# Performance work log

Measured on AMD Instinct MI355X. Metric: run time of the kernel, lower is better.

Reference implementation:

```python
import jax, jax.numpy as jnp
import numpy as np

HID = 1024
NH = 4  # heads for GAT conv1 and all attention blocks
FF = 2048
SLOPE = 0.2


def _ln(x, g, b):
    m = x.mean(-1, keepdims=True)
    v = ((x - m) ** 2).mean(-1, keepdims=True)
    return (x - m) / jnp.sqrt(v + 1e-5) * g + b


def _mha(q, k, v, in_w, in_b, out_w, out_b, nh):
    # q:[B,Lq,E], k/v:[B,Lk,E]; torch MultiheadAttention math (eval mode)
    B, Lq, E = q.shape
    hd = E // nh
    wq, wk, wv = jnp.split(in_w, 3, axis=0)
    bq, bk, bv = jnp.split(in_b, 3)
    qh = (q @ wq.T + bq).reshape(B, Lq, nh, hd)
    kh = (k @ wk.T + bk).reshape(B, -1, nh, hd)
    vh = (v @ wv.T + bv).reshape(B, -1, nh, hd)
    s = jnp.einsum('bqhd,bkhd->bhqk', qh, kh) / jnp.sqrt(jnp.asarray(hd, q.dtype))
    a = jax.nn.softmax(s, axis=-1)
    o = jnp.einsum('bhqk,bkhd->bqhd', a, vh).reshape(B, Lq, E)
    return o @ out_w.T + out_b


def _gatv2(x, edge_index, w_l, b_l, w_r, b_r, att, bias, heads, out_ch):
    # PyG GATv2Conv, flow='target_to_source': i (aggregation dst) = edge_index[0], j = edge_index[1]
    n = x.shape[0]
    dst = edge_index[0]
    src = edge_index[1]
    x_l = (x @ w_l + b_l).reshape(n, heads, out_ch)
    x_r = (x @ w_r + b_r).reshape(n, heads, out_ch)
    msg = x_l[src]                                   # [E,H,C] gathered source features
    e = jax.nn.leaky_relu(msg + x_r[dst], SLOPE)     # [E,H,C]
    alpha = (e * att).sum(-1)                        # [E,H]
    amax = jax.ops.segment_max(alpha, dst, num_segments=n)
    alpha = jnp.exp(alpha - amax[dst])
    denom = jax.ops.segment_sum(alpha, dst, num_segments=n)
    alpha = alpha / (denom[dst] + 1e-16)
    out = jax.ops.segment_sum(msg * alpha[..., None], dst, num_segments=n)
    return out.reshape(n, heads * out_ch) + bias


def setup_inputs() -> dict:
    key = jax.random.key(0)
    ks = iter(jax.random.split(key, 64))
    N, DF, B, L, E_rand = 8000, 768, 32, 14, 96000
    w = lambda *s: jax.random.normal(next(ks), s, jnp.float32) * 0.02
    z = lambda *s: jnp.zeros(s, jnp.float32)
    o = lambda *s: jnp.ones(s, jnp.float32)
    ei = jax.random.randint(next(ks), (2, E_rand), 0, N, jnp.int32)
    self_loops = jnp.tile(jnp.arange(N, dtype=jnp.int32)[None, :], (2, 1))
    inp = {
        'img_feat': jax.random.normal(next(ks), (B, HID), jnp.float32),
        'node_features': jax.random.normal(next(ks), (N, DF), jnp.float32),
        'edge_index': jnp.concatenate([ei, self_loops], axis=1),
        'target_idx': jax.random.randint(next(ks), (L,), 0, N, jnp.int32),
        # GATv2 conv1: 768 -> 4 heads x 256
        'gat1_wl': w(DF, HID), 'gat1_bl': z(HID), 'gat1_wr': w(DF, HID), 'gat1_br': z(HID),
        'gat1_att': w(NH, HID // NH), 'gat1_bias': z(HID),
        # GATv2 conv2: 1024 -> 1 head x 1024
        'gat2_wl': w(HID, HID), 'gat2_bl': z(HID), 'gat2_wr': w(HID, HID), 'gat2_br': z(HID),
        'gat2_att': w(1, HID), 'gat2_bias': z(HID),
        # cross-modal MHA + FFN layer
        'xa_in_w': w(3 * HID, HID), 'xa_in_b': z(3 * HID), 'xa_out_w': w(HID, HID), 'xa_out_b': z(HID),
        'xl_l1_w': w(FF, HID), 'xl_l1_b': z(FF), 'xl_l2_w': w(HID, FF), 'xl_l2_b': z(HID),
        'xl_n1_g': o(HID), 'xl_n1_b': z(HID), 'xl_n2_g': o(HID), 'xl_n2_b': z(HID),
        # 2-layer TransformerEncoder (stacked leading dim = layer)
        'enc_in_w': w(2, 3 * HID, HID), 'enc_in_b': z(2, 3 * HID),
        'enc_out_w': w(2, HID, HID), 'enc_out_b': z(2, HID),
        'enc_l1_w': w(2, FF, HID), 'enc_l1_b': z(2, FF),
        'enc_l2_w': w(2, HID, FF), 'enc_l2_b': z(2, HID),
        'enc_n1_g': o(2, HID), 'enc_n1_b': z(2, HID),
        'enc_n2_g': o(2, HID), 'enc_n2_b': z(2, HID),
        'cls_w': w(1, HID), 'cls_b': z(1),
    }
    return inp


def reference(img_feat, node_features, edge_index, target_idx,
              gat1_wl, gat1_bl, gat1_wr, gat1_br, gat1_att, gat1_bias,
              gat2_wl, gat2_bl, gat2_wr, gat2_br, gat2_att, gat2_bias,
              xa_in_w, xa_in_b, xa_out_w, xa_out_b,
              xl_l1_w, xl_l1_b, xl_l2_w, xl_l2_b, xl_n1_g, xl_n1_b, xl_n2_g, xl_n2_b,
              enc_in_w, enc_in_b, enc_out_w, enc_out_b, enc_l1_w, enc_l1_b, enc_l2_w, enc_l2_b,
              enc_n1_g, enc_n1_b, enc_n2_g, enc_n2_b, cls_w, cls_b):
    x = _gatv2(node_features, edge_index, gat1_wl, gat1_bl, gat1_wr, gat1_br, gat1_att, gat1_bias, NH, HID // NH)
    x = jax.nn.leaky_relu(x, SLOPE)
    x = _gatv2(x, edge_index, gat2_wl, gat2_bl, gat2_wr, gat2_br, gat2_att, gat2_bias, 1, HID)
    t = x[target_idx]                                  # [L, HID]
    B = img_feat.shape[0]
    L = t.shape[0]
    q = jnp.broadcast_to(t[None], (B, L, HID))
    kv = img_feat[:, None, :]                          # [B, 1, HID]
    attn = _mha(q, kv, kv, xa_in_w, xa_in_b, xa_out_w, xa_out_b, NH)
    src = _ln(t[None] + attn, xl_n1_g, xl_n1_b)
    ff = jax.nn.relu(src @ xl_l1_w.T + xl_l1_b) @ xl_l2_w.T + xl_l2_b
    src = _ln(src + ff, xl_n2_g, xl_n2_b)
    for i in range(2):  # TransformerEncoder, post-norm, relu, eval mode
        a = _mha(src, src, src, enc_in_w[i], enc_in_b[i], enc_out_w[i], enc_out_b[i], NH)
        src = _ln(src + a, enc_n1_g[i], enc_n1_b[i])
        f = jax.nn.relu(src @ enc_l1_w[i].T + enc_l1_b[i]) @ enc_l2_w[i].T + enc_l2_b[i]
        src = _ln(src + f, enc_n2_g[i], enc_n2_b[i])
    return (src @ cls_w.T + cls_b)[..., 0]             # [B, L]
```

## Files before the change

kernel.cpp:

```cpp
#include <hip/hip_runtime.h>
#include <hip/hip_bf16.h>

typedef __bf16 bf16;
typedef bf16 bf16x8 __attribute__((ext_vector_type(8)));
typedef bf16 bf16x4 __attribute__((ext_vector_type(4)));
typedef float f32x4 __attribute__((ext_vector_type(4)));

#define HID 1024
#define FFD 2048

typedef __attribute__((address_space(3))) void lds_void;
typedef const __attribute__((address_space(1))) void gm_void;

__device__ __forceinline__ void gload_lds16(const bf16* g, bf16* l)
{
    __builtin_amdgcn_global_load_lds((gm_void*)g, (lds_void*)l, 16, 0, 0);
}

__global__ __launch_bounds__(256) void cvt_bf16_kernel(
    const float* __restrict__ src, bf16* __restrict__ dst, long n)
{
    long i = ((long)blockIdx.x * 256 + threadIdx.x) * 4;
    if (i >= n) return;
    float4 f = *(const float4*)&src[i];
    bf16x4 v = {(bf16)f.x, (bf16)f.y, (bf16)f.z, (bf16)f.w};
    *(bf16x4*)&dst[i] = v;
}

__global__ __launch_bounds__(256) void cvt_t_bf16_kernel(
    const float* __restrict__ in, bf16* __restrict__ out, int R, int C)
{
    __shared__ bf16 tile[32][33];
    const int c0 = blockIdx.x * 32, r0 = blockIdx.y * 32;
    const int tx = threadIdx.x & 31, ty = threadIdx.x >> 5;
#pragma unroll
    for (int i = ty; i < 32; i += 8)
        tile[i][tx] = (bf16)in[(long)(r0 + i) * C + c0 + tx];
    __syncthreads();
#pragma unroll
    for (int i = ty; i < 32; i += 8)
        out[(long)(c0 + i) * R + r0 + tx] = tile[tx][i];
}

template <int ACT, int OUTBF16>
__global__ __launch_bounds__(256) void gemm_bf16_kernel(
    const bf16* __restrict__ A, const bf16* __restrict__ B,
    const float* __restrict__ bias, void* __restrict__ Cp,
    int M, int N, int K, int NB)
{
    const int total = gridDim.x;
    const int h = blockIdx.x;
    const int t = (total % 8 == 0) ? ((h & 7) * (total >> 3) + (h >> 3)) : h;
    const int bn = t % NB, bm = t / NB;

    const int tid  = threadIdx.x;
    const int lane = tid & 63, wave = tid >> 6;
    const int wr   = wave >> 1, wc = wave & 1;

    __shared__ bf16 As[128][32];
    __shared__ bf16 Bs[128][32];

    f32x4 acc[4][4] = {};

    const int srow = wave * 16 + (lane >> 2);
    const int scol = (lane & 3) << 3;
    const long ga0 = (long)min(bm * 128 + srow,      M - 1) * K + scol;
    const long ga1 = (long)min(bm * 128 + srow + 64, M - 1) * K + scol;
    const long gb0 = (long)(bn * 128 + srow)      * K + scol;
    const long gb1 = (long)(bn * 128 + srow + 64) * K + scol;
    bf16* ldsA0 = &As[0][0] + wave * 512;
    bf16* ldsA1 = &As[0][0] + 2048 + wave * 512;
    bf16* ldsB0 = &Bs[0][0] + wave * 512;
    bf16* ldsB1 = &Bs[0][0] + 2048 + wave * 512;

    const int quad = lane >> 4;
    const int mr   = lane & 15;
    const int kf   = quad * 8;

    for (int k0 = 0; k0 < K; k0 += 32) {
        gload_lds16(A + ga0 + k0, ldsA0);
        gload_lds16(A + ga1 + k0, ldsA1);
        gload_lds16(B + gb0 + k0, ldsB0);
        gload_lds16(B + gb1 + k0, ldsB1);
        __syncthreads();

        bf16x8 af[4], bfr[4];
#pragma unroll
        for (int i = 0; i < 4; ++i) af[i]  = *(const bf16x8*)&As[wr * 64 + i * 16 + mr][kf];
#pragma unroll
        for (int j = 0; j < 4; ++j) bfr[j] = *(const bf16x8*)&Bs[wc * 64 + j * 16 + mr][kf];
#pragma unroll
        for (int i = 0; i < 4; ++i)
#pragma unroll
            for (int j = 0; j < 4; ++j)
                acc[i][j] = __builtin_amdgcn_mfma_f32_16x16x32_bf16(af[i], bfr[j], acc[i][j], 0, 0, 0);
        __syncthreads();
    }

    const int crow = quad * 4;
#pragma unroll
    for (int i = 0; i < 4; ++i) {
#pragma unroll
        for (int j = 0; j < 4; ++j) {
            const int   col = bn * 128 + wc * 64 + j * 16 + mr;
            const float bv  = bias[col];
#pragma unroll
            for (int r = 0; r < 4; ++r) {
                const int row = bm * 128 + wr * 64 + i * 16 + crow + r;
                if (row < M) {
                    float v = acc[i][j][r] + bv;
                    if (ACT == 1) v = fmaxf(v, 0.f);
                    if (OUTBF16) ((bf16*)Cp)[(long)row * N + col] = (bf16)v;
                    else         ((float*)Cp)[(long)row * N + col] = v;
                }
            }
        }
    }
}

template <int KS>
__global__ __launch_bounds__(256) void gemm_sk_kernel(
    const float* __restrict__ A, const float* __restrict__ Bt,
    float* __restrict__ part, int M, int N, int K)
{
    const int tid  = threadIdx.x;
    const int bn   = blockIdx.x, bm = blockIdx.y, kz = blockIdx.z;
    const int lane = tid & 63, wave = tid >> 6;
    const int wr   = wave >> 1, wc = wave & 1;

    __shared__ bf16 As[128][40];
    __shared__ bf16 Bs[128][40];

    f32x4 acc[4][4] = {};

    const int  lr = tid >> 2;
    const int  lc = (tid & 3) << 3;
    const long a0 = (long)min(bm * 128 + lr,      M - 1) * K;
    const long a1 = (long)min(bm * 128 + lr + 64, M - 1) * K;
    const long b0 = (long)(bn * 128 + lr)      * K;
    const long b1 = (long)(bn * 128 + lr + 64) * K;

    const int quad = lane >> 4;
    const int mr   = lane & 15;
    const int kf   = quad * 8;

    const int Kc   = K / KS;
    const int kbeg = kz * Kc, kend = kbeg + Kc;

    float4 ra[4], rb[4];
    auto load_chunk = [&](int k0) {
        ra[0] = *(const float4*)&A[a0 + k0 + lc];
        ra[1] = *(const float4*)&A[a0 + k0 + lc + 4];
        ra[2] = *(const float4*)&A[a1 + k0 + lc];
        ra[3] = *(const float4*)&A[a1 + k0 + lc + 4];
        rb[0] = *(const float4*)&Bt[b0 + k0 + lc];
        rb[1] = *(const float4*)&Bt[b0 + k0 + lc + 4];
        rb[2] = *(const float4*)&Bt[b1 + k0 + lc];
        rb[3] = *(const float4*)&Bt[b1 + k0 + lc + 4];
    };

    load_chunk(kbeg);
    for (int k0 = kbeg; k0 < kend; k0 += 32) {
        {
            bf16x8 v0 = {(bf16)ra[0].x,(bf16)ra[0].y,(bf16)ra[0].z,(bf16)ra[0].w,
                         (bf16)ra[1].x,(bf16)ra[1].y,(bf16)ra[1].z,(bf16)ra[1].w};
            *(bf16x8*)&As[lr][lc] = v0;
            bf16x8 v1 = {(bf16)ra[2].x,(bf16)ra[2].y,(bf16)ra[2].z,(bf16)ra[2].w,
                         (bf16)ra[3].x,(bf16)ra[3].y,(bf16)ra[3].z,(bf16)ra[3].w};
            *(bf16x8*)&As[lr + 64][lc] = v1;
            bf16x8 v2 = {(bf16)rb[0].x,(bf16)rb[0].y,(bf16)rb[0].z,(bf16)rb[0].w,
                         (bf16)rb[1].x,(bf16)rb[1].y,(bf16)rb[1].z,(bf16)rb[1].w};
            *(bf16x8*)&Bs[lr][lc] = v2;
            bf16x8 v3 = {(bf16)rb[2].x,(bf16)rb[2].y,(bf16)rb[2].z,(bf16)rb[2].w,
                         (bf16)rb[3].x,(bf16)rb[3].y,(bf16)rb[3].z,(bf16)rb[3].w};
            *(bf16x8*)&Bs[lr + 64][lc] = v3;
        }
        __syncthreads();
        if (k0 + 32 < kend) load_chunk(k0 + 32);

        bf16x8 af[4], bfr[4];
#pragma unroll
        for (int i = 0; i < 4; ++i) af[i]  = *(const bf16x8*)&As[wr * 64 + i * 16 + mr][kf];
#pragma unroll
        for (int j = 0; j < 4; ++j) bfr[j] = *(const bf16x8*)&Bs[wc * 64 + j * 16 + mr][kf];
#pragma unroll
        for (int i = 0; i < 4; ++i)
#pragma unroll
            for (int j = 0; j < 4; ++j)
                acc[i][j] = __builtin_amdgcn_mfma_f32_16x16x32_bf16(af[i], bfr[j], acc[i][j], 0, 0, 0);
        __syncthreads();
    }

    const int crow = quad * 4;
    float* dst = part + (size_t)kz * M * N;
#pragma unroll
    for (int i = 0; i < 4; ++i) {
#pragma unroll
        for (int j = 0; j < 4; ++j) {
            const int col = bn * 128 + wc * 64 + j * 16 + mr;
#pragma unroll
            for (int r = 0; r < 4; ++r) {
                const int row = bm * 128 + wr * 64 + i * 16 + crow + r;
                if (row < M) dst[(long)row * N + col] = acc[i][j][r];
            }
        }
    }
}

template <int ACT, int KS>
__global__ __launch_bounds__(256) void sk_reduce_kernel(
    const float* __restrict__ part, const float* __restrict__ bias,
    float* __restrict__ C, long MN, int N)
{
    long i = ((long)blockIdx.x * 256 + threadIdx.x) * 4;
    if (i >= MN) return;
    float4 s = *(const float4*)&part[i];
#pragma unroll
    for (int k = 1; k < KS; ++k) {
        float4 p = *(const float4*)&part[(size_t)k * MN + i];
        s.x += p.x; s.y += p.y; s.z += p.z; s.w += p.w;
    }
    const int col = (int)(i % N);
    float4 bv = *(const float4*)&bias[col];
    s.x += bv.x; s.y += bv.y; s.z += bv.z; s.w += bv.w;
    if (ACT) {
        s.x = fmaxf(s.x, 0.f); s.y = fmaxf(s.y, 0.f);
        s.z = fmaxf(s.z, 0.f); s.w = fmaxf(s.w, 0.f);
    }
    *(float4*)&C[i] = s;
}

__device__ __forceinline__ void ln_finish(float v[4], int c0, const float* g,
                                          const float* beta, float* outrow)
{
    float s1 = v[0] + v[1] + v[2] + v[3];
    float s2 = v[0] * v[0] + v[1] * v[1] + v[2] * v[2] + v[3] * v[3];
    __shared__ float red[8];
    for (int o = 32; o; o >>= 1) { s1 += __shfl_down(s1, o); s2 += __shfl_down(s2, o); }
    const int wave = threadIdx.x >> 6, lane = threadIdx.x & 63;
    if (lane == 0) { red[wave] = s1; red[4 + wave] = s2; }
    __syncthreads();
    if (threadIdx.x == 0) {
        red[0] += red[1] + red[2] + red[3];
        red[4] += red[5] + red[6] + red[7];
    }
    __syncthreads();
    const float mean = red[0] * (1.f / HID);
    const float var  = fmaxf(red[4] * (1.f / HID) - mean * mean, 0.f);
    const float rstd = rsqrtf(var + 1e-5f);
#pragma unroll
    for (int k = 0; k < 4; ++k) {
        int c = c0 + k;
        outrow[c] = (v[k] - mean) * rstd * g[c] + beta[c];
    }
}

template <int KS>
__global__ __launch_bounds__(256) void sk_reduce_ln_kernel(
    const float* __restrict__ part, const float* __restrict__ bias,
    float* __restrict__ srcio, const float* __restrict__ g,
    const float* __restrict__ beta, long MN)
{
    const long row = blockIdx.x;
    const int c0 = threadIdx.x * 4;
    const long base = row * HID + c0;
    float4 s = *(const float4*)&part[base];
#pragma unroll
    for (int k = 1; k < KS; ++k) {
        float4 p = *(const float4*)&part[(size_t)k * MN + base];
        s.x += p.x; s.y += p.y; s.z += p.z; s.w += p.w;
    }
    float4 bv = *(const float4*)&bias[c0];
    float4 rv = *(const float4*)&srcio[base];
    float v[4] = {s.x + bv.x + rv.x, s.y + bv.y + rv.y,
                  s.z + bv.z + rv.z, s.w + bv.w + rv.w};
    ln_finish(v, c0, g, beta, srcio + row * HID);
}

__global__ void zero_i32_kernel(int* __restrict__ p, int n)
{
    int i = blockIdx.x * 256 + threadIdx.x;
    if (i < n) p[i] = 0;
}

__global__ void hist_kernel(const int* __restrict__ ei, int E, int* __restrict__ deg)
{
    int e = blockIdx.x * 256 + threadIdx.x;
    if (e < E) atomicAdd(&deg[ei[e]], 1);
}

__global__ void scan_kernel(const int* __restrict__ deg, int* __restrict__ rowstart,
                            int* __restrict__ cursor, int n)
{
    __shared__ int sm[1024];
    __shared__ int carry;
    if (threadIdx.x == 0) carry = 0;
    __syncthreads();
    for (int base = 0; base < n; base += 1024) {
        int i = base + threadIdx.x;
        int v = (i < n) ? deg[i] : 0;
        sm[threadIdx.x] = v;
        __syncthreads();
        for (int off = 1; off < 1024; off <<= 1) {
            int t = (threadIdx.x >= off) ? sm[threadIdx.x - off] : 0;
            __syncthreads();
            sm[threadIdx.x] += t;
            __syncthreads();
        }
        if (i < n) { int ex = carry + sm[threadIdx.x] - v; rowstart[i] = ex; cursor[i] = ex; }
        __syncthreads();
        if (threadIdx.x == 0) carry += sm[1023];
        __syncthreads();
    }
    if (threadIdx.x == 0) rowstart[n] = carry;
}

__global__ void scatter_kernel(const int* __restrict__ ei, int E,
                               int* __restrict__ cursor, int* __restrict__ eidx)
{
    int e = blockIdx.x * 256 + threadIdx.x;
    if (e < E) { int p = atomicAdd(&cursor[ei[e]], 1); eidx[p] = e; }
}

template <int NH, int LRELU, int OUTBF16>
__global__ __launch_bounds__(256) void gat_wave_kernel(
    const bf16* __restrict__ xl, const bf16* __restrict__ xr,
    const float* __restrict__ att,
    const int* __restrict__ ei, const int* __restrict__ rowstart,
    const int* __restrict__ eidx, const float* __restrict__ bias,
    void* __restrict__ outp, int E, int Nn)
{
    const int wave = threadIdx.x >> 6, lane = threadIdx.x & 63;
    const int n = blockIdx.x * 4 + wave;
    if (n >= Nn) return;

    const int rs = rowstart[n];
    int deg = rowstart[n + 1] - rs;
    if (deg > 128) deg = 128;

    int my_src = ei[E + eidx[min(rs + lane, E - 1)]];
    int my_src2 = 0;
    if (deg > 64) my_src2 = ei[E + eidx[min(rs + 64 + lane, E - 1)]];

    const int c0 = lane * 16;
    float xrf[16], av[16];
    {
        bf16x8 r0 = *(const bf16x8*)&xr[(long)n * HID + c0];
        bf16x8 r1 = *(const bf16x8*)&xr[(long)n * HID + c0 + 8];
#pragma unroll
        for (int t = 0; t < 8; ++t) { xrf[t] = (float)r0[t]; xrf[8 + t] = (float)r1[t]; }
        float4 t0 = *(const float4*)&att[c0],     t1 = *(const float4*)&att[c0 + 4];
        float4 t2 = *(const float4*)&att[c0 + 8], t3 = *(const float4*)&att[c0 + 12];
        av[0]=t0.x; av[1]=t0.y; av[2]=t0.z;  av[3]=t0.w;
        av[4]=t1.x; av[5]=t1.y; av[6]=t1.z;  av[7]=t1.w;
        av[8]=t2.x; av[9]=t2.y; av[10]=t2.z; av[11]=t2.w;
        av[12]=t3.x; av[13]=t3.y; av[14]=t3.z; av[15]=t3.w;
    }

    float m = -1e30f, s = 0.f;
    float acc[16];
#pragma unroll
    for (int t = 0; t < 16; ++t) acc[t] = 0.f;

    int sj = __shfl(my_src, 0);
    bf16x8 na0 = *(const bf16x8*)&xl[(long)sj * HID + c0];
    bf16x8 na1 = *(const bf16x8*)&xl[(long)sj * HID + c0 + 8];

    for (int j = 0; j < deg; ++j) {
        bf16x8 x0 = na0, x1 = na1;
        if (j + 1 < deg) {
            int msrc = (j + 1 < 64) ? my_src : my_src2;
            int sn = __shfl(msrc, (j + 1) & 63);
            na0 = *(const bf16x8*)&xl[(long)sn * HID + c0];
            na1 = *(const bf16x8*)&xl[(long)sn * HID + c0 + 8];
        }
        float xf[16];
#pragma unroll
        for (int t = 0; t < 8; ++t) { xf[t] = (float)x0[t]; xf[8 + t] = (float)x1[t]; }
        float partial = 0.f;
#pragma unroll
        for (int t = 0; t < 16; ++t) {
            float v = xf[t] + xrf[t];
            v = v > 0.f ? v : 0.2f * v;
            partial += v * av[t];
        }
        const int RW = (NH == 4) ? 16 : 64;
#pragma unroll
        for (int o = 1; o < RW; o <<= 1) partial += __shfl_xor(partial, o);
        float mn = fmaxf(m, partial);
        float f = __expf(m - mn);
        float p = __expf(partial - mn);
        s = s * f + p;
#pragma unroll
        for (int t = 0; t < 16; ++t) acc[t] = acc[t] * f + p * xf[t];
        m = mn;
    }

    const float dinv = 1.f / (s + 1e-16f);
    float bv[16];
    {
        float4 t0 = *(const float4*)&bias[c0],     t1 = *(const float4*)&bias[c0 + 4];
        float4 t2 = *(const float4*)&bias[c0 + 8], t3 = *(const float4*)&bias[c0 + 12];
        bv[0]=t0.x; bv[1]=t0.y; bv[2]=t0.z;  bv[3]=t0.w;
        bv[4]=t1.x; bv[5]=t1.y; bv[6]=t1.z;  bv[7]=t1.w;
        bv[8]=t2.x; bv[9]=t2.y; bv[10]=t2.z; bv[11]=t2.w;
        bv[12]=t3.x; bv[13]=t3.y; bv[14]=t3.z; bv[15]=t3.w;
    }
    float ov[16];
#pragma unroll
    for (int t = 0; t < 16; ++t) {
        float v = acc[t] * dinv + bv[t];
        if (LRELU) v = v > 0.f ? v : 0.2f * v;
        ov[t] = v;
    }
    if (OUTBF16) {
        bf16x8 w0, w1;
#pragma unroll
        for (int t = 0; t < 8; ++t) { w0[t] = (bf16)ov[t]; w1[t] = (bf16)ov[8 + t]; }
        *(bf16x8*)&((bf16*)outp)[(long)n * HID + c0] = w0;
        *(bf16x8*)&((bf16*)outp)[(long)n * HID + c0 + 8] = w1;
    } else {
        float* op = (float*)outp + (long)n * HID + c0;
#pragma unroll
        for (int t = 0; t < 4; ++t) {
            float4 w = {ov[t * 4], ov[t * 4 + 1], ov[t * 4 + 2], ov[t * 4 + 3]};
            *(float4*)&op[t * 4] = w;
        }
    }
}

__global__ __launch_bounds__(256) void ln_cross_kernel(
    const float* __restrict__ x2, const int* __restrict__ tidx,
    const float* __restrict__ attnb, const float* __restrict__ g,
    const float* __restrict__ beta, float* __restrict__ out, int L)
{
    const int row = blockIdx.x;
    const int b = row / L, l = row - b * L;
    const long tr = (long)tidx[l] * HID, ar = (long)b * HID;
    const int c0 = threadIdx.x * 4;
    float v[4];
#pragma unroll
    for (int k = 0; k < 4; ++k)
        v[k] = x2[tr + c0 + k] + attnb[ar + c0 + k];
    ln_finish(v, c0, g, beta, out + (long)row * HID);
}

__global__ __launch_bounds__(256) void self_attn_kernel(
    const float* __restrict__ qkv, float* __restrict__ out, int L)
{
    const int b = blockIdx.x >> 2, h = blockIdx.x & 3;
    const int tid = threadIdx.x;
    __shared__ float q[16][256], kk[16][256], vv[16][256];
    __shared__ float sc[16][16];
    for (int i = tid; i < L * 256; i += 256) {
        const int l = i >> 8, d = i & 255;
        const long rb = (long)(b * L + l) * 3072 + h * 256 + d;
        q[l][d]  = qkv[rb];
        kk[l][d] = qkv[rb + 1024];
        vv[l][d] = qkv[rb + 2048];
    }
    __syncthreads();
    if (tid < L * L) {
        const int l1 = tid / L, l2 = tid - l1 * L;
        float s = 0.f;
        for (int d = 0; d < 256; ++d) s += q[l1][d] * kk[l2][d];
        sc[l1][l2] = s * 0.0625f;
    }
    __syncthreads();
    if (tid < L) {
        float mx = -1e30f;
        for (int j = 0; j < L; ++j) mx = fmaxf(mx, sc[tid][j]);
        float ssum = 0.f;
        for (int j = 0; j < L; ++j) { float e = expf(sc[tid][j] - mx); sc[tid][j] = e; ssum += e; }
        const float inv = 1.f / ssum;
        for (int j = 0; j < L; ++j) sc[tid][j] *= inv;
    }
    __syncthreads();
    for (int l1 = 0; l1 < L; ++l1) {
        float a = 0.f;
        for (int l2 = 0; l2 < L; ++l2) a += sc[l1][l2] * vv[l2][tid];
        out[(long)(b * L + l1) * HID + h * 256 + tid] = a;
    }
}

__global__ __launch_bounds__(256) void cls_kernel(
    const float* __restrict__ src, const float* __restrict__ w,
    const float* __restrict__ b, float* __restrict__ out, int rows)
{
    const int row = blockIdx.x * 4 + (threadIdx.x >> 6);
    const int lane = threadIdx.x & 63;
    if (row >= rows) return;
    float s = 0.f;
    for (int c = lane; c < HID; c += 64) s += src[(long)row * HID + c] * w[c];
    for (int o = 32; o; o >>= 1) s += __shfl_down(s, o);
    if (lane == 0) out[row] = s + b[0];
}

extern "C" void kernel_launch(void* const* d_in, const int* in_sizes, int n_in,
                              void* d_out, int out_size, void* d_ws, size_t ws_size,
                              hipStream_t stream)
{
    const float* img_feat      = (const float*)d_in[0];
    const float* node_features = (const float*)d_in[1];
    const int*   edge_index    = (const int*)d_in[2];
    const int*   target_idx    = (const int*)d_in[3];
    const float* gat1_wl  = (const float*)d_in[4];
    const float* gat1_bl  = (const float*)d_in[5];
    const float* gat1_wr  = (const float*)d_in[6];
    const float* gat1_br  = (const float*)d_in[7];
    const float* gat1_att = (const float*)d_in[8];
    const float* gat1_bias= (const float*)d_in[9];
    const float* gat2_wl  = (const float*)d_in[10];
    const float* gat2_bl  = (const float*)d_in[11];
    const float* gat2_wr  = (const float*)d_in[12];
    const float* gat2_br  = (const float*)d_in[13];
    const float* gat2_att = (const float*)d_in[14];
    const float* gat2_bias= (const float*)d_in[15];
    const float* xa_in_w  = (const float*)d_in[16];
    const float* xa_in_b  = (const float*)d_in[17];
    const float* xa_out_w = (const float*)d_in[18];
    const float* xa_out_b = (const float*)d_in[19];
    const float* xl_l1_w  = (const float*)d_in[20];
    const float* xl_l1_b  = (const float*)d_in[21];
    const float* xl_l2_w  = (const float*)d_in[22];
    const float* xl_l2_b  = (const float*)d_in[23];
    const float* xl_n1_g  = (const float*)d_in[24];
    const float* xl_n1_b  = (const float*)d_in[25];
    const float* xl_n2_g  = (const float*)d_in[26];
    const float* xl_n2_b  = (const float*)d_in[27];
    const float* enc_in_w = (const float*)d_in[28];
    const float* enc_in_b = (const float*)d_in[29];
    const float* enc_out_w= (const float*)d_in[30];
    const float* enc_out_b= (const float*)d_in[31];
    const float* enc_l1_w = (const float*)d_in[32];
    const float* enc_l1_b = (const float*)d_in[33];
    const float* enc_l2_w = (const float*)d_in[34];
    const float* enc_l2_b = (const float*)d_in[35];
    const float* enc_n1_g = (const float*)d_in[36];
    const float* enc_n1_b = (const float*)d_in[37];
    const float* enc_n2_g = (const float*)d_in[38];
    const float* enc_n2_b = (const float*)d_in[39];
    const float* cls_w    = (const float*)d_in[40];
    const float* cls_b    = (const float*)d_in[41];

    const int DF = in_sizes[4] / HID;
    const int Nn = in_sizes[1] / DF;
    const int E  = in_sizes[2] / 2;
    const int L  = in_sizes[3];
    const int B  = in_sizes[0] / HID;
    const int R  = B * L;

    char* basep = (char*)d_ws;
    size_t off = 0;
    auto alloc = [&](size_t bytes) -> char* {
        char* r = basep + off; off += (bytes + 255) & ~(size_t)255; return r;
    };
    size_t regA_need = 0;
    {
        auto sz = [&](size_t b) { regA_need += (b + 255) & ~(size_t)255; };
        sz((size_t)Nn * DF * 2); sz((size_t)DF * HID * 2); sz((size_t)DF * HID * 2);
        sz((size_t)HID * HID * 2); sz((size_t)HID * HID * 2); sz((size_t)Nn * HID * 2);
    }
    size_t regA_bytes = regA_need > (size_t)Nn * HID * 4 ? regA_need : (size_t)Nn * HID * 4;
    char* regionA = alloc(regA_bytes);
    {
        size_t aoff = 0;
        auto allocA = [&](size_t bytes) -> char* {
            char* r = regionA + aoff; aoff += (bytes + 255) & ~(size_t)255; return r;
        };
        bf16* nfb  = (bf16*)allocA((size_t)Nn * DF * 2);
        bf16* w1lT = (bf16*)allocA((size_t)DF * HID * 2);
        bf16* w1rT = (bf16*)allocA((size_t)DF * HID * 2);
        bf16* w2lT = (bf16*)allocA((size_t)HID * HID * 2);
        bf16* w2rT = (bf16*)allocA((size_t)HID * HID * 2);
        bf16* x1   = (bf16*)allocA((size_t)Nn * HID * 2);

        float* x2  = (float*)regionA;

        bf16* xlb = (bf16*)alloc((size_t)Nn * HID * 2);
        bf16* xrb = (bf16*)alloc((size_t)Nn * HID * 2);
        int*   deg      = (int*)alloc((size_t)Nn * 4);
        int*   rowstart = (int*)alloc((size_t)(Nn + 1) * 4);
        int*   cursor   = (int*)alloc((size_t)(Nn + 1) * 4);
        int*   eidx     = (int*)alloc((size_t)E * 4);
        float* skpart   = (float*)alloc((size_t)8 * R * 3 * HID * 4);

        char* qb = (char*)xlb; size_t qoff = 0;
        auto alloc2 = [&](size_t bytes) -> char* {
            char* r = qb + qoff; qoff += (bytes + 255) & ~(size_t)255; return r;
        };
        float* vproj  = (float*)alloc2((size_t)B * HID * 4);
        float* attnb  = (float*)alloc2((size_t)B * HID * 4);
        float* srcbuf = (float*)alloc2((size_t)R * HID * 4);
        float* h1buf  = (float*)alloc2((size_t)R * FFD * 4);
        float* ffbuf  = (float*)alloc2((size_t)R * HID * 4);
        float* qkvbuf = (float*)alloc2((size_t)R * 3 * HID * 4);

        const int gE  = (E + 255) / 256;
        const int gMn = (Nn + 127) / 128;
        const long MNr = (long)R * HID;

        auto gemm_sk4 = [&](const float* A, const float* Bt, const float* bias,
                            float* C, int M, int N, int K, int act) {
            gemm_sk_kernel<4><<<dim3(N / 128, (M + 127) / 128, 4), 256, 0, stream>>>(
                A, Bt, skpart, M, N, K);
            long MN = (long)M * N;
            int g = (int)((MN / 4 + 255) / 256);
            if (act) sk_reduce_kernel<1,4><<<g, 256, 0, stream>>>(skpart, bias, C, MN, N);
            else     sk_reduce_kernel<0,4><<<g, 256, 0, stream>>>(skpart, bias, C, MN, N);
        };
        auto gemm_sk8 = [&](const float* A, const float* Bt, const float* bias,
                            float* C, int M, int N, int K, int act) {
            gemm_sk_kernel<8><<<dim3(N / 128, (M + 127) / 128, 8), 256, 0, stream>>>(
                A, Bt, skpart, M, N, K);
            long MN = (long)M * N;
            int g = (int)((MN / 4 + 255) / 256);
            if (act) sk_reduce_kernel<1,8><<<g, 256, 0, stream>>>(skpart, bias, C, MN, N);
            else     sk_reduce_kernel<0,8><<<g, 256, 0, stream>>>(skpart, bias, C, MN, N);
        };
        auto gemm_sk8_ln = [&](const float* A, const float* Bt, const float* bias,
                               float* srcio, const float* g, const float* beta, int K) {
            gemm_sk_kernel<8><<<dim3(HID / 128, (R + 127) / 128, 8), 256, 0, stream>>>(
                A, Bt, skpart, R, HID, K);
            sk_reduce_ln_kernel<8><<<R, 256, 0, stream>>>(skpart, bias, srcio, g, beta, MNr);
        };

        zero_i32_kernel<<<(Nn + 255) / 256, 256, 0, stream>>>(deg, Nn);
        hist_kernel<<<gE, 256, 0, stream>>>(edge_index, E, deg);
        scan_kernel<<<1, 1024, 0, stream>>>(deg, rowstart, cursor, Nn);
        scatter_kernel<<<gE, 256, 0, stream>>>(edge_index, E, cursor, eidx);

        cvt_bf16_kernel<<<(int)(((long)Nn * DF / 4 + 255) / 256), 256, 0, stream>>>(
            node_features, nfb, (long)Nn * DF);
        cvt_t_bf16_kernel<<<dim3(HID / 32, DF / 32), 256, 0, stream>>>(gat1_wl, w1lT, DF, HID);
        cvt_t_bf16_kernel<<<dim3(HID / 32, DF / 32), 256, 0, stream>>>(gat1_wr, w1rT, DF, HID);
        cvt_t_bf16_kernel<<<dim3(HID / 32, HID / 32), 256, 0, stream>>>(gat2_wl, w2lT, HID, HID);
        cvt_t_bf16_kernel<<<dim3(HID / 32, HID / 32), 256, 0, stream>>>(gat2_wr, w2rT, HID, HID);

        gemm_bf16_kernel<0,1><<<8 * gMn, 256, 0, stream>>>(nfb, w1lT, gat1_bl, xlb, Nn, HID, DF, 8);
        gemm_bf16_kernel<0,1><<<8 * gMn, 256, 0, stream>>>(nfb, w1rT, gat1_br, xrb, Nn, HID, DF, 8);
        gat_wave_kernel<4,1,1><<<(Nn + 3) / 4, 256, 0, stream>>>(
            xlb, xrb, gat1_att, edge_index, rowstart, eidx, gat1_bias, x1, E, Nn);

        gemm_bf16_kernel<0,1><<<8 * gMn, 256, 0, stream>>>(x1, w2lT, gat2_bl, xlb, Nn, HID, HID, 8);
        gemm_bf16_kernel<0,1><<<8 * gMn, 256, 0, stream>>>(x1, w2rT, gat2_br, xrb, Nn, HID, HID, 8);
        gat_wave_kernel<1,0,0><<<(Nn + 3) / 4, 256, 0, stream>>>(
            xlb, xrb, gat2_att, edge_index, rowstart, eidx, gat2_bias, x2, E, Nn);

        gemm_sk8(img_feat, xa_in_w + (size_t)2 * HID * HID, xa_in_b + 2 * HID, vproj, B, HID, HID, 0);
        gemm_sk8(vproj, xa_out_w, xa_out_b, attnb, B, HID, HID, 0);
        ln_cross_kernel<<<R, 256, 0, stream>>>(x2, target_idx, attnb, xl_n1_g, xl_n1_b, srcbuf, L);

        gemm_sk4(srcbuf, xl_l1_w, xl_l1_b, h1buf, R, FFD, HID, 1);
        gemm_sk8_ln(h1buf, xl_l2_w, xl_l2_b, srcbuf, xl_n2_g, xl_n2_b, FFD);

        for (int i = 0; i < 2; ++i) {
            gemm_sk4(srcbuf, enc_in_w + (size_t)i * 3 * HID * HID, enc_in_b + i * 3 * HID,
                     qkvbuf, R, 3 * HID, HID, 0);
            self_attn_kernel<<<B * 4, 256, 0, stream>>>(qkvbuf, ffbuf, L);
            gemm_sk8_ln(ffbuf, enc_out_w + (size_t)i * HID * HID, enc_out_b + i * HID,
                        srcbuf, enc_n1_g + i * HID, enc_n1_b + i * HID, HID);
            gemm_sk4(srcbuf, enc_l1_w + (size_t)i * FFD * HID, enc_l1_b + i * FFD,
                     h1buf, R, FFD, HID, 1);
            gemm_sk8_ln(h1buf, enc_l2_w + (size_t)i * HID * FFD, enc_l2_b + i * HID,
                        srcbuf, enc_n2_g + i * HID, enc_n2_b + i * HID, FFD);
        }

        cls_kernel<<<(R + 3) / 4, 256, 0, stream>>>(srcbuf, cls_w, cls_b, (float*)d_out, R);
    }
}
```

Before: 696.6 us.

## Compute GAT layers only on target nodes' 2-hop neighborhood

Instead of running both GATv2 layers over all 8000 nodes, the code marks the target nodes, their in-neighbors and the neighbors' in-neighbors, compacts these lists, and runs the projections and attention only on the gathered subset. It also batches the weight conversions into single launches, fuses the layer-2 left and right projections into one GEMM, and switches the transformer GEMMs to bf16 inputs with bf16 outputs. This removes most of the GNN GEMM and aggregation work, which is valid because only target rows feed the output. In exchange, per-node edge lists are capped at 128 entries, which would silently drop edges for high-degree nodes, and the multi-pass atomic compaction makes row order nondeterministic.

Result: faster. 621.7 us (-10.8%).

```diff
diff --git a/kernel.cpp b/kernel.cpp
--- a/kernel.cpp
+++ b/kernel.cpp
@@ -17,42 +17,139 @@
     __builtin_amdgcn_global_load_lds((gm_void*)g, (lds_void*)l, 16, 0, 0);
 }
 
-__global__ __launch_bounds__(256) void cvt_bf16_kernel(
-    const float* __restrict__ src, bf16* __restrict__ dst, long n)
-{
-    long i = ((long)blockIdx.x * 256 + threadIdx.x) * 4;
-    if (i >= n) return;
-    float4 f = *(const float4*)&src[i];
+struct CvtEnt { const float* src; bf16* dst; int b0; };
+struct CvtArgs { CvtEnt e[14]; int n; };
+
+__global__ __launch_bounds__(256) void batch_cvt_kernel(CvtArgs a)
+{
+    int k = 0;
+    while (k + 1 < a.n && (int)blockIdx.x >= a.e[k + 1].b0) ++k;
+    const long i = ((long)((int)blockIdx.x - a.e[k].b0) * 256 + threadIdx.x) * 4;
+    float4 f = *(const float4*)&a.e[k].src[i];
     bf16x4 v = {(bf16)f.x, (bf16)f.y, (bf16)f.z, (bf16)f.w};
-    *(bf16x4*)&dst[i] = v;
-}
-
-__global__ __launch_bounds__(256) void cvt_t_bf16_kernel(
-    const float* __restrict__ in, bf16* __restrict__ out, int R, int C)
+    *(bf16x4*)&a.e[k].dst[i] = v;
+}
+
+struct CvtTEnt { const float* src; bf16* dst; int R, C, b0; };
+struct CvtTArgs { CvtTEnt e[4]; int n; };
+
+__global__ __launch_bounds__(256) void batch_cvt_t_kernel(CvtTArgs a)
 {
     __shared__ bf16 tile[32][33];
-    const int c0 = blockIdx.x * 32, r0 = blockIdx.y * 32;
+    int k = 0;
+    while (k + 1 < a.n && (int)blockIdx.x >= a.e[k + 1].b0) ++k;
+    const CvtTEnt en = a.e[k];
+    const int lb = (int)blockIdx.x - en.b0;
+    const int CB = en.C >> 5;
+    const int c0 = (lb % CB) * 32, r0 = (lb / CB) * 32;
     const int tx = threadIdx.x & 31, ty = threadIdx.x >> 5;
 #pragma unroll
     for (int i = ty; i < 32; i += 8)
-        tile[i][tx] = (bf16)in[(long)(r0 + i) * C + c0 + tx];
+        tile[i][tx] = (bf16)en.src[(long)(r0 + i) * en.C + c0 + tx];
     __syncthreads();
 #pragma unroll
     for (int i = ty; i < 32; i += 8)
-        out[(long)(c0 + i) * R + r0 + tx] = tile[tx][i];
-}
-
-template <int ACT, int OUTBF16>
-__global__ __launch_bounds__(256) void gemm_bf16_kernel(
+        en.dst[(long)(c0 + i) * en.R + r0 + tx] = tile[tx][i];
+}
+
+struct GemmDesc {
+    const bf16* A; const bf16* B; const float* bias; void* C;
+    int M, N, K, NB; const int* cnt; int act, outbf16;
+};
+
+__device__ __forceinline__ void gemm_body(const GemmDesc g, int h, int total,
+                                          bf16 (*As)[32], bf16 (*Bs)[32])
+{
+    const int t = (total % 8 == 0) ? ((h & 7) * (total >> 3) + (h >> 3)) : h;
+    const int bn = t % g.NB, bm = t / g.NB;
+    int Meff = g.cnt ? *g.cnt : g.M;
+    if (Meff <= 0) return;
+    if (bm * 128 >= Meff) return;
+
+    const int tid  = threadIdx.x;
+    const int lane = tid & 63, wave = tid >> 6;
+    const int wr   = wave >> 1, wc = wave & 1;
+
+    f32x4 acc[4][4] = {};
+
+    const int srow = wave * 16 + (lane >> 2);
+    const int scol = (lane & 3) << 3;
+    const long ga0 = (long)min(bm * 128 + srow,      Meff - 1) * g.K + scol;
+    const long ga1 = (long)min(bm * 128 + srow + 64, Meff - 1) * g.K + scol;
+    const long gb0 = (long)(bn * 128 + srow)      * g.K + scol;
+    const long gb1 = (long)(bn * 128 + srow + 64) * g.K + scol;
+    bf16* ldsA0 = &As[0][0] + wave * 512;
+    bf16* ldsA1 = &As[0][0] + 2048 + wave * 512;
+    bf16* ldsB0 = &Bs[0][0] + wave * 512;
+    bf16* ldsB1 = &Bs[0][0] + 2048 + wave * 512;
+
+    const int quad = lane >> 4;
+    const int mr   = lane & 15;
+    const int kf   = quad * 8;
+
+    for (int k0 = 0; k0 < g.K; k0 += 32) {
+        gload_lds16(g.A + ga0 + k0, ldsA0);
+        gload_lds16(g.A + ga1 + k0, ldsA1);
+        gload_lds16(g.B + gb0 + k0, ldsB0);
+        gload_lds16(g.B + gb1 + k0, ldsB1);
+        __syncthreads();
+
+        bf16x8 af[4], bfr[4];
+#pragma unroll
+        for (int i = 0; i < 4; ++i) af[i]  = *(const bf16x8*)&As[wr * 64 + i * 16 + mr][kf];
+#pragma unroll
+        for (int j = 0; j < 4; ++j) bfr[j] = *(const bf16x8*)&Bs[wc * 64 + j * 16 + mr][kf];
+#pragma unroll
+        for (int i = 0; i < 4; ++i)
+#pragma unroll
+            for (int j = 0; j < 4; ++j)
+                acc[i][j] = __builtin_amdgcn_mfma_f32_16x16x32_bf16(af[i], bfr[j], acc[i][j], 0, 0, 0);
+        __syncthreads();
+    }
+
+    const int crow = quad * 4;
+#pragma unroll
+    for (int i = 0; i < 4; ++i) {
+#pragma unroll
+        for (int j = 0; j < 4; ++j) {
+            const int   col = bn * 128 + wc * 64 + j * 16 + mr;
+            const float bv  = g.bias[col];
+#pragma unroll
+            for (int r = 0; r < 4; ++r) {
+                const int row = bm * 128 + wr * 64 + i * 16 + crow + r;
+                if (row < Meff) {
+                    float v = acc[i][j][r] + bv;
+                    if (g.act) v = fmaxf(v, 0.f);
+                    if (g.outbf16) ((bf16*)g.C)[(long)row * g.N + col] = (bf16)v;
+                    else           ((float*)g.C)[(long)row * g.N + col] = v;
+                }
+            }
+        }
+    }
+}
+
+__global__ __launch_bounds__(256) void gemm_one_kernel(GemmDesc g)
+{
+    __shared__ bf16 As[128][32];
+    __shared__ bf16 Bs[128][32];
+    gemm_body(g, blockIdx.x, gridDim.x, As, Bs);
+}
+
+__global__ __launch_bounds__(256) void gemm_dual_kernel(GemmDesc g0, int n0,
+                                                        GemmDesc g1, int n1)
+{
+    __shared__ bf16 As[128][32];
+    __shared__ bf16 Bs[128][32];
+    if ((int)blockIdx.x < n0) gemm_body(g0, blockIdx.x, n0, As, Bs);
+    else                      gemm_body(g1, (int)blockIdx.x - n0, n1, As, Bs);
+}
+
+template <int KS>
+__global__ __launch_bounds__(256) void gemm_bsk_kernel(
     const bf16* __restrict__ A, const bf16* __restrict__ B,
-    const float* __restrict__ bias, void* __restrict__ Cp,
-    int M, int N, int K, int NB)
-{
-    const int total = gridDim.x;
-    const int h = blockIdx.x;
-    const int t = (total % 8 == 0) ? ((h & 7) * (total >> 3) + (h >> 3)) : h;
-    const int bn = t % NB, bm = t / NB;
-
+    float* __restrict__ part, int M, int N, int K)
+{
+    const int bn = blockIdx.x, bm = blockIdx.y, kz = blockIdx.z;
     const int tid  = threadIdx.x;
     const int lane = tid & 63, wave = tid >> 6;
     const int wr   = wave >> 1, wc = wave & 1;
@@ -77,7 +174,8 @@
     const int mr   = lane & 15;
     const int kf   = quad * 8;
 
-    for (int k0 = 0; k0 < K; k0 += 32) {
+    const int Kc = K / KS, kbeg = kz * Kc, kend = kbeg + Kc;
+    for (int k0 = kbeg; k0 < kend; k0 += 32) {
         gload_lds16(A + ga0 + k0, ldsA0);
         gload_lds16(A + ga1 + k0, ldsA1);
         gload_lds16(B + gb0 + k0, ldsB0);
@@ -97,102 +195,8 @@
         __syncthreads();
     }
 
+    float* dst = part + (size_t)kz * M * N;
     const int crow = quad * 4;
-#pragma unroll
-    for (int i = 0; i < 4; ++i) {
-#pragma unroll
-        for (int j = 0; j < 4; ++j) {
-            const int   col = bn * 128 + wc * 64 + j * 16 + mr;
-            const float bv  = bias[col];
-#pragma unroll
-            for (int r = 0; r < 4; ++r) {
-                const int row = bm * 128 + wr * 64 + i * 16 + crow + r;
-                if (row < M) {
-                    float v = acc[i][j][r] + bv;
-                    if (ACT == 1) v = fmaxf(v, 0.f);
-                    if (OUTBF16) ((bf16*)Cp)[(long)row * N + col] = (bf16)v;
-                    else         ((float*)Cp)[(long)row * N + col] = v;
-                }
-            }
-        }
-    }
-}
-
-template <int KS>
-__global__ __launch_bounds__(256) void gemm_sk_kernel(
-    const float* __restrict__ A, const float* __restrict__ Bt,
-    float* __restrict__ part, int M, int N, int K)
-{
-    const int tid  = threadIdx.x;
-    const int bn   = blockIdx.x, bm = blockIdx.y, kz = blockIdx.z;
-    const int lane = tid & 63, wave = tid >> 6;
-    const int wr   = wave >> 1, wc = wave & 1;
-
-    __shared__ bf16 As[128][40];
-    __shared__ bf16 Bs[128][40];
-
-    f32x4 acc[4][4] = {};
-
-    const int  lr = tid >> 2;
-    const int  lc = (tid & 3) << 3;
-    const long a0 = (long)min(bm * 128 + lr,      M - 1) * K;
-    const long a1 = (long)min(bm * 128 + lr + 64, M - 1) * K;
-    const long b0 = (long)(bn * 128 + lr)      * K;
-    const long b1 = (long)(bn * 128 + lr + 64) * K;
-
-    const int quad = lane >> 4;
-    const int mr   = lane & 15;
-    const int kf   = quad * 8;
-
-    const int Kc   = K / KS;
-    const int kbeg = kz * Kc, kend = kbeg + Kc;
-
-    float4 ra[4], rb[4];
-    auto load_chunk = [&](int k0) {
-        ra[0] = *(const float4*)&A[a0 + k0 + lc];
-        ra[1] = *(const float4*)&A[a0 + k0 + lc + 4];
-        ra[2] = *(const float4*)&A[a1 + k0 + lc];
-        ra[3] = *(const float4*)&A[a1 + k0 + lc + 4];
-        rb[0] = *(const float4*)&Bt[b0 + k0 + lc];
-        rb[1] = *(const float4*)&Bt[b0 + k0 + lc + 4];
-        rb[2] = *(const float4*)&Bt[b1 + k0 + lc];
-        rb[3] = *(const float4*)&Bt[b1 + k0 + lc + 4];
-    };
-
-    load_chunk(kbeg);
-    for (int k0 = kbeg; k0 < kend; k0 += 32) {
-        {
-            bf16x8 v0 = {(bf16)ra[0].x,(bf16)ra[0].y,(bf16)ra[0].z,(bf16)ra[0].w,
-                         (bf16)ra[1].x,(bf16)ra[1].y,(bf16)ra[1].z,(bf16)ra[1].w};
-            *(bf16x8*)&As[lr][lc] = v0;
-            bf16x8 v1 = {(bf16)ra[2].x,(bf16)ra[2].y,(bf16)ra[2].z,(bf16)ra[2].w,
-                         (bf16)ra[3].x,(bf16)ra[3].y,(bf16)ra[3].z,(bf16)ra[3].w};
-            *(bf16x8*)&As[lr + 64][lc] = v1;
-            bf16x8 v2 = {(bf16)rb[0].x,(bf16)rb[0].y,(bf16)rb[0].z,(bf16)rb[0].w,
-                         (bf16)rb[1].x,(bf16)rb[1].y,(bf16)rb[1].z,(bf16)rb[1].w};
-            *(bf16x8*)&Bs[lr][lc] = v2;
-            bf16x8 v3 = {(bf16)rb[2].x,(bf16)rb[2].y,(bf16)rb[2].z,(bf16)rb[2].w,
-                         (bf16)rb[3].x,(bf16)rb[3].y,(bf16)rb[3].z,(bf16)rb[3].w};
-            *(bf16x8*)&Bs[lr + 64][lc] = v3;
-        }
-        __syncthreads();
-        if (k0 + 32 < kend) load_chunk(k0 + 32);
-
-        bf16x8 af[4], bfr[4];
-#pragma unroll
-        for (int i = 0; i < 4; ++i) af[i]  = *(const bf16x8*)&As[wr * 64 + i * 16 + mr][kf];
-#pragma unroll
-        for (int j = 0; j < 4; ++j) bfr[j] = *(const bf16x8*)&Bs[wc * 64 + j * 16 + mr][kf];
-#pragma unroll
-        for (int i = 0; i < 4; ++i)
-#pragma unroll
-            for (int j = 0; j < 4; ++j)
-                acc[i][j] = __builtin_amdgcn_mfma_f32_16x16x32_bf16(af[i], bfr[j], acc[i][j], 0, 0, 0);
-        __syncthreads();
-    }
-
-    const int crow = quad * 4;
-    float* dst = part + (size_t)kz * M * N;
 #pragma unroll
     for (int i = 0; i < 4; ++i) {
 #pragma unroll
@@ -208,9 +212,9 @@
 }
 
 template <int ACT, int KS>
-__global__ __launch_bounds__(256) void sk_reduce_kernel(
+__global__ __launch_bounds__(256) void sk_reduce_b16_kernel(
     const float* __restrict__ part, const float* __restrict__ bias,
-    float* __restrict__ C, long MN, int N)
+    bf16* __restrict__ C, long MN, int N)
 {
     long i = ((long)blockIdx.x * 256 + threadIdx.x) * 4;
     if (i >= MN) return;
@@ -227,11 +231,13 @@
         s.x = fmaxf(s.x, 0.f); s.y = fmaxf(s.y, 0.f);
         s.z = fmaxf(s.z, 0.f); s.w = fmaxf(s.w, 0.f);
     }
-    *(float4*)&C[i] = s;
+    bf16x4 v = {(bf16)s.x, (bf16)s.y, (bf16)s.z, (bf16)s.w};
+    *(bf16x4*)&C[i] = v;
 }
 
 __device__ __forceinline__ void ln_finish(float v[4], int c0, const float* g,
-                                          const float* beta, float* outrow)
+                                          const float* beta, float* outrow,
+                                          bf16* outb)
 {
     float s1 = v[0] + v[1] + v[2] + v[3];
     float s2 = v[0] * v[0] + v[1] * v[1] + v[2] * v[2] + v[3] * v[3];
@@ -251,15 +257,17 @@
 #pragma unroll
     for (int k = 0; k < 4; ++k) {
         int c = c0 + k;
-        outrow[c] = (v[k] - mean) * rstd * g[c] + beta[c];
+        float o = (v[k] - mean) * rstd * g[c] + beta[c];
+        outrow[c] = o;
+        outb[c] = (bf16)o;
     }
 }
 
 template <int KS>
 __global__ __launch_bounds__(256) void sk_reduce_ln_kernel(
     const float* __restrict__ part, const float* __restrict__ bias,
-    float* __restrict__ srcio, const float* __restrict__ g,
-    const float* __restrict__ beta, long MN)
+    float* __restrict__ srcio, bf16* __restrict__ srcb,
+    const float* __restrict__ g, const float* __restrict__ beta, long MN)
 {
     const long row = blockIdx.x;
     const int c0 = threadIdx.x * 4;
@@ -274,79 +282,107 @@
     float4 rv = *(const float4*)&srcio[base];
     float v[4] = {s.x + bv.x + rv.x, s.y + bv.y + rv.y,
                   s.z + bv.z + rv.z, s.w + bv.w + rv.w};
-    ln_finish(v, c0, g, beta, srcio + row * HID);
-}
-
-__global__ void zero_i32_kernel(int* __restrict__ p, int n)
+    ln_finish(v, c0, g, beta, srcio + row * HID, srcb + row * HID);
+}
+
+__global__ void zero_prep_kernel(int* __restrict__ zp, int Z,
+                                 const float* __restrict__ bl,
+                                 const float* __restrict__ br,
+                                 float* __restrict__ bias2)
 {
     int i = blockIdx.x * 256 + threadIdx.x;
-    if (i < n) p[i] = 0;
-}
-
-__global__ void hist_kernel(const int* __restrict__ ei, int E, int* __restrict__ deg)
-{
+    if (i < Z) zp[i] = 0;
+    int j = i - Z;
+    if (j >= 0 && j < HID) bias2[j] = bl[j];
+    else if (j >= HID && j < 2 * HID) bias2[j] = br[j - HID];
+}
+
+__global__ __launch_bounds__(256) void pass0_kernel(
+    const int* __restrict__ ei, int E, const int* __restrict__ tgt, int L,
+    int* __restrict__ cntE0, int* __restrict__ srcs0, int* __restrict__ f1)
+{
+    __shared__ int ts[16];
+    if ((int)threadIdx.x < L) ts[threadIdx.x] = tgt[threadIdx.x];
+    __syncthreads();
+    if (blockIdx.x == 0 && (int)threadIdx.x < L) f1[ts[threadIdx.x]] = 1;
     int e = blockIdx.x * 256 + threadIdx.x;
-    if (e < E) atomicAdd(&deg[ei[e]], 1);
-}
-
-__global__ void scan_kernel(const int* __restrict__ deg, int* __restrict__ rowstart,
-                            int* __restrict__ cursor, int n)
-{
-    __shared__ int sm[1024];
-    __shared__ int carry;
-    if (threadIdx.x == 0) carry = 0;
-    __syncthreads();
-    for (int base = 0; base < n; base += 1024) {
-        int i = base + threadIdx.x;
-        int v = (i < n) ? deg[i] : 0;
-        sm[threadIdx.x] = v;
-        __syncthreads();
-        for (int off = 1; off < 1024; off <<= 1) {
-            int t = (threadIdx.x >= off) ? sm[threadIdx.x - off] : 0;
-            __syncthreads();
-            sm[threadIdx.x] += t;
-            __syncthreads();
+    if (e >= E) return;
+    int d = ei[e];
+    int c = -1;
+    for (int l = 0; l < L; ++l) if (ts[l] == d) { c = l; break; }
+    if (c < 0) return;
+    int s = atomicAdd(&cntE0[c], 1);
+    if (s < 128) { int sr = ei[E + e]; srcs0[c * 128 + s] = sr; f1[sr] = 1; }
+}
+
+__global__ __launch_bounds__(256) void pass1_kernel(
+    const int* __restrict__ ei, int E, const int* __restrict__ f1,
+    const int* __restrict__ map1, int* __restrict__ cntE1,
+    int* __restrict__ srcs1, int* __restrict__ f2)
+{
+    int e = blockIdx.x * 256 + threadIdx.x;
+    if (e >= E) return;
+    int d = ei[e];
+    if (!f1[d]) return;
+    int c = map1[d];
+    int s = atomicAdd(&cntE1[c], 1);
+    if (s < 128) { int sr = ei[E + e]; srcs1[c * 128 + s] = sr; f2[sr] = 1; }
+}
+
+__global__ __launch_bounds__(256) void compact_kernel(
+    const int* __restrict__ flags, int* __restrict__ map, int* __restrict__ list,
+    int* __restrict__ cnt, int n)
+{
+    int i = blockIdx.x * 256 + threadIdx.x;
+    if (i < n && flags[i]) {
+        int p = atomicAdd(cnt, 1);
+        list[p] = i;
+        map[i] = p;
+    }
+}
+
+__global__ __launch_bounds__(256) void gather2_kernel(
+    const float* __restrict__ nf,
+    bf16* __restrict__ nf2c, const int* __restrict__ list2, const int* __restrict__ cnt2,
+    bf16* __restrict__ nf1c, const int* __restrict__ list1, const int* __restrict__ cnt1,
+    int DF)
+{
+    int bid = blockIdx.x;
+    const int* list; int cnt, stride; bf16* dst;
+    if (bid < 2048) { list = list2; cnt = *cnt2; dst = nf2c; stride = 2048; }
+    else { bid -= 2048; list = list1; cnt = *cnt1; dst = nf1c; stride = 512; }
+    for (int r = bid; r < cnt; r += stride) {
+        const long i = (long)list[r] * DF;
+        const long o = (long)r * DF;
+        for (int c = threadIdx.x * 4; c < DF; c += 1024) {
+            float4 f = *(const float4*)&nf[i + c];
+            bf16x4 v = {(bf16)f.x, (bf16)f.y, (bf16)f.z, (bf16)f.w};
+            *(bf16x4*)&dst[o + c] = v;
         }
-        if (i < n) { int ex = carry + sm[threadIdx.x] - v; rowstart[i] = ex; cursor[i] = ex; }
-        __syncthreads();
-        if (threadIdx.x == 0) carry += sm[1023];
-        __syncthreads();
-    }
-    if (threadIdx.x == 0) rowstart[n] = carry;
-}
-
-__global__ void scatter_kernel(const int* __restrict__ ei, int E,
-                               int* __restrict__ cursor, int* __restrict__ eidx)
-{
-    int e = blockIdx.x * 256 + threadIdx.x;
-    if (e < E) { int p = atomicAdd(&cursor[ei[e]], 1); eidx[p] = e; }
-}
-
-template <int NH, int LRELU, int OUTBF16>
-__global__ __launch_bounds__(256) void gat_wave_kernel(
+    }
+}
+
+__global__ __launch_bounds__(256) void gat_wave1_kernel(
     const bf16* __restrict__ xl, const bf16* __restrict__ xr,
-    const float* __restrict__ att,
-    const int* __restrict__ ei, const int* __restrict__ rowstart,
-    const int* __restrict__ eidx, const float* __restrict__ bias,
-    void* __restrict__ outp, int E, int Nn)
+    const float* __restrict__ att, const int* __restrict__ srcs,
+    const int* __restrict__ cntE, const int* __restrict__ srcmap,
+    const int* __restrict__ cntp, const float* __restrict__ bias,
+    bf16* __restrict__ outp)
 {
     const int wave = threadIdx.x >> 6, lane = threadIdx.x & 63;
-    const int n = blockIdx.x * 4 + wave;
-    if (n >= Nn) return;
-
-    const int rs = rowstart[n];
-    int deg = rowstart[n + 1] - rs;
-    if (deg > 128) deg = 128;
-
-    int my_src = ei[E + eidx[min(rs + lane, E - 1)]];
+    const int w = blockIdx.x * 4 + wave;
+    if (w >= *cntp) return;
+    int deg = min(cntE[w], 128);
+    const int base = w * 128;
+    int my_src = srcmap[srcs[base + min(lane, deg - 1)]];
     int my_src2 = 0;
-    if (deg > 64) my_src2 = ei[E + eidx[min(rs + 64 + lane, E - 1)]];
+    if (deg > 64) my_src2 = srcmap[srcs[base + 64 + min(lane, deg - 65)]];
 
     const int c0 = lane * 16;
     float xrf[16], av[16];
     {
-        bf16x8 r0 = *(const bf16x8*)&xr[(long)n * HID + c0];
-        bf16x8 r1 = *(const bf16x8*)&xr[(long)n * HID + c0 + 8];
+        bf16x8 r0 = *(const bf16x8*)&xr[(long)w * HID + c0];
+        bf16x8 r1 = *(const bf16x8*)&xr[(long)w * HID + c0 + 8];
 #pragma unroll
         for (int t = 0; t < 8; ++t) { xrf[t] = (float)r0[t]; xrf[8 + t] = (float)r1[t]; }
         float4 t0 = *(const float4*)&att[c0],     t1 = *(const float4*)&att[c0 + 4];
@@ -384,9 +420,8 @@
             v = v > 0.f ? v : 0.2f * v;
             partial += v * av[t];
         }
-        const int RW = (NH == 4) ? 16 : 64;
-#pragma unroll
-        for (int o = 1; o < RW; o <<= 1) partial += __shfl_xor(partial, o);
+#pragma unroll
+        for (int o = 1; o < 16; o <<= 1) partial += __shfl_xor(partial, o);
         float mn = fmaxf(m, partial);
         float f = __expf(m - mn);
         float p = __expf(partial - mn);
@@ -406,58 +441,139 @@
         bv[8]=t2.x; bv[9]=t2.y; bv[10]=t2.z; bv[11]=t2.w;
         bv[12]=t3.x; bv[13]=t3.y; bv[14]=t3.z; bv[15]=t3.w;
     }
-    float ov[16];
+    bf16x8 w0, w1;
 #pragma unroll
     for (int t = 0; t < 16; ++t) {
         float v = acc[t] * dinv + bv[t];
-        if (LRELU) v = v > 0.f ? v : 0.2f * v;
-        ov[t] = v;
-    }
-    if (OUTBF16) {
-        bf16x8 w0, w1;
-#pragma unroll
-        for (int t = 0; t < 8; ++t) { w0[t] = (bf16)ov[t]; w1[t] = (bf16)ov[8 + t]; }
-        *(bf16x8*)&((bf16*)outp)[(long)n * HID + c0] = w0;
-        *(bf16x8*)&((bf16*)outp)[(long)n * HID + c0 + 8] = w1;
-    } else {
-        float* op = (float*)outp + (long)n * HID + c0;
-#pragma unroll
-        for (int t = 0; t < 4; ++t) {
-            float4 w = {ov[t * 4], ov[t * 4 + 1], ov[t * 4 + 2], ov[t * 4 + 3]};
-            *(float4*)&op[t * 4] = w;
+        v = v > 0.f ? v : 0.2f * v;
+        if (t < 8) w0[t] = (bf16)v; else w1[t - 8] = (bf16)v;
+    }
+    *(bf16x8*)&outp[(long)w * HID + c0] = w0;
+    *(bf16x8*)&outp[(long)w * HID + c0 + 8] = w1;
+}
+
+__global__ __launch_bounds__(256) void gat_wave2_kernel(
+    const bf16* __restrict__ x12, const float* __restrict__ att,
+    const int* __restrict__ tgt, int L, const int* __restrict__ srcs,
+    const int* __restrict__ cntE, const int* __restrict__ map1,
+    const float* __restrict__ bias, float* __restrict__ outp)
+{
+    const int wave = threadIdx.x >> 6, lane = threadIdx.x & 63;
+    const int w = blockIdx.x * 4 + wave;
+    if (w >= L) return;
+    const int n = tgt[w];
+    int c = 0;
+    for (int l = 0; l < L; ++l) if (tgt[l] == n) { c = l; break; }
+    int deg = min(cntE[c], 128);
+    const int base = c * 128;
+    int my_src = map1[srcs[base + min(lane, deg - 1)]];
+    int my_src2 = 0;
+    if (deg > 64) my_src2 = map1[srcs[base + 64 + min(lane, deg - 65)]];
+
+    const int c0 = lane * 16;
+    const long LD = 2 * HID;
+    float xrf[16], av[16];
+    {
+        const long xrr = (long)map1[n] * LD + HID + c0;
+        bf16x8 r0 = *(const bf16x8*)&x12[xrr];
+        bf16x8 r1 = *(const bf16x8*)&x12[xrr + 8];
+#pragma unroll
+        for (int t = 0; t < 8; ++t) { xrf[t] = (float)r0[t]; xrf[8 + t] = (float)r1[t]; }
+        float4 t0 = *(const float4*)&att[c0],     t1 = *(const float4*)&att[c0 + 4];
+        float4 t2 = *(const float4*)&att[c0 + 8], t3 = *(const float4*)&att[c0 + 12];
+        av[0]=t0.x; av[1]=t0.y; av[2]=t0.z;  av[3]=t0.w;
+        av[4]=t1.x; av[5]=t1.y; av[6]=t1.z;  av[7]=t1.w;
+        av[8]=t2.x; av[9]=t2.y; av[10]=t2.z; av[11]=t2.w;
+        av[12]=t3.x; av[13]=t3.y; av[14]=t3.z; av[15]=t3.w;
+    }
+
+    float m = -1e30f, s = 0.f;
+    float acc[16];
+#pragma unroll
+    for (int t = 0; t < 16; ++t) acc[t] = 0.f;
+
+    int sj = __shfl(my_src, 0);
+    bf16x8 na0 = *(const bf16x8*)&x12[(long)sj * LD + c0];
+    bf16x8 na1 = *(const bf16x8*)&x12[(long)sj * LD + c0 + 8];
+
+    for (int j = 0; j < deg; ++j) {
+        bf16x8 x0 = na0, x1 = na1;
+        if (j + 1 < deg) {
+            int msrc = (j + 1 < 64) ? my_src : my_src2;
+            int sn = __shfl(msrc, (j + 1) & 63);
+            na0 = *(const bf16x8*)&x12[(long)sn * LD + c0];
+            na1 = *(const bf16x8*)&x12[(long)sn * LD + c0 + 8];
         }
+        float xf[16];
+#pragma unroll
+        for (int t = 0; t < 8; ++t) { xf[t] = (float)x0[t]; xf[8 + t] = (float)x1[t]; }
+        float partial = 0.f;
+#pragma unroll
+        for (int t = 0; t < 16; ++t) {
+            float v = xf[t] + xrf[t];
+            v = v > 0.f ? v : 0.2f * v;
+            partial += v * av[t];
+        }
+#pragma unroll
+        for (int o = 1; o < 64; o <<= 1) partial += __shfl_xor(partial, o);
+        float mn = fmaxf(m, partial);
+        float f = __expf(m - mn);
+        float p = __expf(partial - mn);
+        s = s * f + p;
+#pragma unroll
+        for (int t = 0; t < 16; ++t) acc[t] = acc[t] * f + p * xf[t];
+        m = mn;
+    }
+
+    const float dinv = 1.f / (s + 1e-16f);
+    float* op = outp + (long)w * HID + c0;
+#pragma unroll
+    for (int t = 0; t < 4; ++t) {
+        float4 b4 = *(const float4*)&bias[c0 + t * 4];
+        float4 wv = {acc[t*4] * dinv + b4.x, acc[t*4+1] * dinv + b4.y,
+                     acc[t*4+2] * dinv + b4.z, acc[t*4+3] * dinv + b4.w};
+        *(float4*)&op[t * 4] = wv;
     }
 }
 
 __global__ __launch_bounds__(256) void ln_cross_kernel(
-    const float* __restrict__ x2, const int* __restrict__ tidx,
-    const float* __restrict__ attnb, const float* __restrict__ g,
-    const float* __restrict__ beta, float* __restrict__ out, int L)
+    const float* __restrict__ x2c, const float* __restrict__ attnb,
+    const float* __restrict__ g, const float* __restrict__ beta,
+    float* __restrict__ out, bf16* __restrict__ outb, int L)
 {
     const int row = blockIdx.x;
     const int b = row / L, l = row - b * L;
-    const long tr = (long)tidx[l] * HID, ar = (long)b * HID;
     const int c0 = threadIdx.x * 4;
     float v[4];
 #pragma unroll
     for (int k = 0; k < 4; ++k)
-        v[k] = x2[tr + c0 + k] + attnb[ar + c0 + k];
-    ln_finish(v, c0, g, beta, out + (long)row * HID);
-}
-
-__global__ __launch_bounds__(256) void self_attn_kernel(
-    const float* __restrict__ qkv, float* __restrict__ out, int L)
+        v[k] = x2c[(long)l * HID + c0 + k] + attnb[(long)b * HID + c0 + k];
+    ln_finish(v, c0, g, beta, out + (long)row * HID, outb + (long)row * HID);
+}
+
+template <int KS>
+__global__ __launch_bounds__(256) void self_attn_sk_kernel(
+    const float* __restrict__ part, const float* __restrict__ bias,
+    bf16* __restrict__ out, int L, int R)
 {
     const int b = blockIdx.x >> 2, h = blockIdx.x & 3;
     const int tid = threadIdx.x;
     __shared__ float q[16][256], kk[16][256], vv[16][256];
     __shared__ float sc[16][16];
+    const size_t PS = (size_t)R * 3 * HID;
     for (int i = tid; i < L * 256; i += 256) {
         const int l = i >> 8, d = i & 255;
-        const long rb = (long)(b * L + l) * 3072 + h * 256 + d;
-        q[l][d]  = qkv[rb];
-        kk[l][d] = qkv[rb + 1024];
-        vv[l][d] = qkv[rb + 2048];
+        const long rb = (long)(b * L + l) * 3 * HID + h * 256 + d;
+        float sq = part[rb], sk = part[rb + HID], sv = part[rb + 2 * HID];
+#pragma unroll
+        for (int k = 1; k < KS; ++k) {
+            sq += part[k * PS + rb];
+            sk += part[k * PS + rb + HID];
+            sv += part[k * PS + rb + 2 * HID];
+        }
+        q[l][d]  = sq + bias[h * 256 + d];
+        kk[l][d] = sk + bias[HID + h * 256 + d];
+        vv[l][d] = sv + bias[2 * HID + h * 256 + d];
     }
     __syncthreads();
     if (tid < L * L) {
@@ -479,7 +595,7 @@
     for (int l1 = 0; l1 < L; ++l1) {
         float a = 0.f;
         for (int l2 = 0; l2 < L; ++l2) a += sc[l1][l2] * vv[l2][tid];
-        out[(long)(b * L + l1) * HID + h * 256 + tid] = a;
+        out[(long)(b * L + l1) * HID + h * 256 + tid] = (bf16)a;
     }
 }
 
@@ -550,122 +666,160 @@
     const int B  = in_sizes[0] / HID;
     const int R  = B * L;
 
+    const int cap1 = ((L * 129 + 127) / 128) * 128;
+    const int gMn1 = cap1 / 128;
+    const int gMn2 = (Nn + 127) / 128;
+
     char* basep = (char*)d_ws;
     size_t off = 0;
     auto alloc = [&](size_t bytes) -> char* {
         char* r = basep + off; off += (bytes + 255) & ~(size_t)255; return r;
     };
-    size_t regA_need = 0;
+
+    bf16* w1lT = (bf16*)alloc((size_t)DF * HID * 2);
+    bf16* w1rT = (bf16*)alloc((size_t)DF * HID * 2);
+    bf16* w2T  = (bf16*)alloc((size_t)2 * HID * HID * 2);
+    float* bias2 = (float*)alloc((size_t)2 * HID * 4);
+
+    bf16* xa_v_b  = (bf16*)alloc((size_t)HID * HID * 2);
+    bf16* xa_o_b  = (bf16*)alloc((size_t)HID * HID * 2);
+    bf16* xl1_b   = (bf16*)alloc((size_t)FFD * HID * 2);
+    bf16* xl2_b   = (bf16*)alloc((size_t)HID * FFD * 2);
+    bf16* ein_b[2], *eout_b[2], *el1_b[2], *el2_b[2];
+    for (int i = 0; i < 2; ++i) {
+        ein_b[i]  = (bf16*)alloc((size_t)3 * HID * HID * 2);
+        eout_b[i] = (bf16*)alloc((size_t)HID * HID * 2);
+        el1_b[i]  = (bf16*)alloc((size_t)FFD * HID * 2);
+        el2_b[i]  = (bf16*)alloc((size_t)HID * FFD * 2);
+    }
+    bf16* imgb = (bf16*)alloc((size_t)B * HID * 2);
+
+    int* zbase = (int*)alloc((size_t)(2 * Nn + cap1 + 32) * 4);
+    int* f1 = zbase;
+    int* f2 = f1 + Nn;
+    int* cntE1 = f2 + Nn;
+    int* cntE0 = cntE1 + cap1;
+    int* cnt1 = cntE0 + 16;
+    int* cnt2 = cnt1 + 1;
+    const int Z = 2 * Nn + cap1 + 18;
+
+    int* map1  = (int*)alloc((size_t)Nn * 4);
+    int* map2  = (int*)alloc((size_t)Nn * 4);
+    int* list1 = (int*)alloc((size_t)cap1 * 4);
+    int* list2 = (int*)alloc((size_t)Nn * 4);
+    int* srcs0 = (int*)alloc((size_t)16 * 128 * 4);
+    int* srcs1 = (int*)alloc((size_t)cap1 * 128 * 4);
+
+    bf16* nf2c = (bf16*)alloc((size_t)Nn * DF * 2);
+    bf16* nf1c = (bf16*)alloc((size_t)cap1 * DF * 2);
+    bf16* xlc  = (bf16*)alloc((size_t)Nn * HID * 2);
+    bf16* xrc  = (bf16*)alloc((size_t)cap1 * HID * 2);
+    bf16* x1c  = (bf16*)alloc((size_t)cap1 * HID * 2);
+    bf16* x12c = (bf16*)alloc((size_t)cap1 * 2 * HID * 2);
+    float* x2c = (float*)alloc((size_t)16 * HID * 4);
+    bf16* vprojb = (bf16*)alloc((size_t)B * HID * 2);
+    float* attnb = (float*)alloc((size_t)B * HID * 4);
+    float* srcbuf = (float*)alloc((size_t)R * HID * 4);
+    bf16*  srcb16 = (bf16*)alloc((size_t)R * HID * 2);
+    bf16*  h1b    = (bf16*)alloc((size_t)R * FFD * 2);
+    bf16*  ffb16  = (bf16*)alloc((size_t)R * HID * 2);
+    float* skpart = (float*)alloc((size_t)4 * R * 3 * HID * 4);
+
+    const int gE = (E + 255) / 256;
+    const long MNr = (long)R * HID;
+
     {
-        auto sz = [&](size_t b) { regA_need += (b + 255) & ~(size_t)255; };
-        sz((size_t)Nn * DF * 2); sz((size_t)DF * HID * 2); sz((size_t)DF * HID * 2);
-        sz((size_t)HID * HID * 2); sz((size_t)HID * HID * 2); sz((size_t)Nn * HID * 2);
-    }
-    size_t regA_bytes = regA_need > (size_t)Nn * HID * 4 ? regA_need : (size_t)Nn * HID * 4;
-    char* regionA = alloc(regA_bytes);
+        CvtTArgs ta; ta.n = 4;
+        int b0 = 0;
+        ta.e[0] = {gat1_wl, w1lT, DF, HID, b0};  b0 += (HID/32)*(DF/32);
+        ta.e[1] = {gat1_wr, w1rT, DF, HID, b0};  b0 += (HID/32)*(DF/32);
+        ta.e[2] = {gat2_wl, w2T,             HID, HID, b0}; b0 += (HID/32)*(HID/32);
+        ta.e[3] = {gat2_wr, w2T + (size_t)HID*HID, HID, HID, b0}; b0 += (HID/32)*(HID/32);
+        batch_cvt_t_kernel<<<b0, 256, 0, stream>>>(ta);
+    }
     {
-        size_t aoff = 0;
-        auto allocA = [&](size_t bytes) -> char* {
-            char* r = regionA + aoff; aoff += (bytes + 255) & ~(size_t)255; return r;
+        CvtArgs ca; int b0 = 0, k = 0;
+        auto add = [&](const float* s, bf16* d, long elems) {
+            ca.e[k++] = {s, d, b0}; b0 += (int)(elems / 1024);
         };
-        bf16* nfb  = (bf16*)allocA((size_t)Nn * DF * 2);
-        bf16* w1lT = (bf16*)allocA((size_t)DF * HID * 2);
-        bf16* w1rT = (bf16*)allocA((size_t)DF * HID * 2);
-        bf16* w2lT = (bf16*)allocA((size_t)HID * HID * 2);
-        bf16* w2rT = (bf16*)allocA((size_t)HID * HID * 2);
-        bf16* x1   = (bf16*)allocA((size_t)Nn * HID * 2);
-
-        float* x2  = (float*)regionA;
-
-        bf16* xlb = (bf16*)alloc((size_t)Nn * HID * 2);
-        bf16* xrb = (bf16*)alloc((size_t)Nn * HID * 2);
-        int*   deg      = (int*)alloc((size_t)Nn * 4);
-        int*   rowstart = (int*)alloc((size_t)(Nn + 1) * 4);
-        int*   cursor   = (int*)alloc((size_t)(Nn + 1) * 4);
-        int*   eidx     = (int*)alloc((size_t)E * 4);
-        float* skpart   = (float*)alloc((size_t)8 * R * 3 * HID * 4);
-
-        char* qb = (char*)xlb; size_t qoff = 0;
-        auto alloc2 = [&](size_t bytes) -> char* {
-            char* r = qb + qoff; qoff += (bytes + 255) & ~(size_t)255; return r;
-        };
-        float* vproj  = (float*)alloc2((size_t)B * HID * 4);
-        float* attnb  = (float*)alloc2((size_t)B * HID * 4);
-        float* srcbuf = (float*)alloc2((size_t)R * HID * 4);
-        float* h1buf  = (float*)alloc2((size_t)R * FFD * 4);
-        float* ffbuf  = (float*)alloc2((size_t)R * HID * 4);
-        float* qkvbuf = (float*)alloc2((size_t)R * 3 * HID * 4);
-
-        const int gE  = (E + 255) / 256;
-        const int gMn = (Nn + 127) / 128;
-        const long MNr = (long)R * HID;
-
-        auto gemm_sk4 = [&](const float* A, const float* Bt, const float* bias,
-                            float* C, int M, int N, int K, int act) {
-            gemm_sk_kernel<4><<<dim3(N / 128, (M + 127) / 128, 4), 256, 0, stream>>>(
-                A, Bt, skpart, M, N, K);
-            long MN = (long)M * N;
-            int g = (int)((MN / 4 + 255) / 256);
-            if (act) sk_reduce_kernel<1,4><<<g, 256, 0, stream>>>(skpart, bias, C, MN, N);
-            else     sk_reduce_kernel<0,4><<<g, 256, 0, stream>>>(skpart, bias, C, MN, N);
-        };
-        auto gemm_sk8 = [&](const float* A, const float* Bt, const float* bias,
-                            float* C, int M, int N, int K, int act) {
-            gemm_sk_kernel<8><<<dim3(N / 128, (M + 127) / 128, 8), 256, 0, stream>>>(
-                A, Bt, skpart, M, N, K);
-            long MN = (long)M * N;
-            int g = (int)((MN / 4 + 255) / 256);
-            if (act) sk_reduce_kernel<1,8><<<g, 256, 0, stream>>>(skpart, bias, C, MN, N);
-            else     sk_reduce_kernel<0,8><<<g, 256, 0, stream>>>(skpart, bias, C, MN, N);
-        };
-        auto gemm_sk8_ln = [&](const float* A, const float* Bt, const float* bias,
-                               float* srcio, const float* g, const float* beta, int K) {
-            gemm_sk_kernel<8><<<dim3(HID / 128, (R + 127) / 128, 8), 256, 0, stream>>>(
-                A, Bt, skpart, R, HID, K);
-            sk_reduce_ln_kernel<8><<<R, 256, 0, stream>>>(skpart, bias, srcio, g, beta, MNr);
-        };
-
-        zero_i32_kernel<<<(Nn + 255) / 256, 256, 0, stream>>>(deg, Nn);
-        hist_kernel<<<gE, 256, 0, stream>>>(edge_index, E, deg);
-        scan_kernel<<<1, 1024, 0, stream>>>(deg, rowstart, cursor, Nn);
-        scatter_kernel<<<gE, 256, 0, stream>>>(edge_index, E, cursor, eidx);
-
-        cvt_bf16_kernel<<<(int)(((long)Nn * DF / 4 + 255) / 256), 256, 0, stream>>>(
-            node_features, nfb, (long)Nn * DF);
-        cvt_t_bf16_kernel<<<dim3(HID / 32, DF / 32), 256, 0, stream>>>(gat1_wl, w1lT, DF, HID);
-        cvt_t_bf16_kernel<<<dim3(HID / 32, DF / 32), 256, 0, stream>>>(gat1_wr, w1rT, DF, HID);
-        cvt_t_bf16_kernel<<<dim3(HID / 32, HID / 32), 256, 0, stream>>>(gat2_wl, w2lT, HID, HID);
-        cvt_t_bf16_kernel<<<dim3(HID / 32, HID / 32), 256, 0, stream>>>(gat2_wr, w2rT, HID, HID);
-
-        gemm_bf16_kernel<0,1><<<8 * gMn, 256, 0, stream>>>(nfb, w1lT, gat1_bl, xlb, Nn, HID, DF, 8);
-        gemm_bf16_kernel<0,1><<<8 * gMn, 256, 0, stream>>>(nfb, w1rT, gat1_br, xrb, Nn, HID, DF, 8);
-        gat_wave_kernel<4,1,1><<<(Nn + 3) / 4, 256, 0, stream>>>(
-            xlb, xrb, gat1_att, edge_index, rowstart, eidx, gat1_bias, x1, E, Nn);
-
-        gemm_bf16_kernel<0,1><<<8 * gMn, 256, 0, stream>>>(x1, w2lT, gat2_bl, xlb, Nn, HID, HID, 8);
-        gemm_bf16_kernel<0,1><<<8 * gMn, 256, 0, stream>>>(x1, w2rT, gat2_br, xrb, Nn, HID, HID, 8);
-        gat_wave_kernel<1,0,0><<<(Nn + 3) / 4, 256, 0, stream>>>(
-            xlb, xrb, gat2_att, edge_index, rowstart, eidx, gat2_bias, x2, E, Nn);
-
-        gemm_sk8(img_feat, xa_in_w + (size_t)2 * HID * HID, xa_in_b + 2 * HID, vproj, B, HID, HID, 0);
-        gemm_sk8(vproj, xa_out_w, xa_out_b, attnb, B, HID, HID, 0);
-        ln_cross_kernel<<<R, 256, 0, stream>>>(x2, target_idx, attnb, xl_n1_g, xl_n1_b, srcbuf, L);
-
-        gemm_sk4(srcbuf, xl_l1_w, xl_l1_b, h1buf, R, FFD, HID, 1);
-        gemm_sk8_ln(h1buf, xl_l2_w, xl_l2_b, srcbuf, xl_n2_g, xl_n2_b, FFD);
-
+        add(img_feat, imgb, (long)B * HID);
+        add(xa_in_w + (size_t)2 * HID * HID, xa_v_b, (long)HID * HID);
+        add(xa_out_w, xa_o_b, (long)HID * HID);
+        add(xl_l1_w, xl1_b, (long)FFD * HID);
+        add(xl_l2_w, xl2_b, (long)HID * FFD);
         for (int i = 0; i < 2; ++i) {
-            gemm_sk4(srcbuf, enc_in_w + (size_t)i * 3 * HID * HID, enc_in_b + i * 3 * HID,
-                     qkvbuf, R, 3 * HID, HID, 0);
-            self_attn_kernel<<<B * 4, 256, 0, stream>>>(qkvbuf, ffbuf, L);
-            gemm_sk8_ln(ffbuf, enc_out_w + (size_t)i * HID * HID, enc_out_b + i * HID,
-                        srcbuf, enc_n1_g + i * HID, enc_n1_b + i * HID, HID);
-            gemm_sk4(srcbuf, enc_l1_w + (size_t)i * FFD * HID, enc_l1_b + i * FFD,
-                     h1buf, R, FFD, HID, 1);
-            gemm_sk8_ln(h1buf, enc_l2_w + (size_t)i * HID * FFD, enc_l2_b + i * HID,
-                        srcbuf, enc_n2_g + i * HID, enc_n2_b + i * HID, FFD);
+            add(enc_in_w  + (size_t)i * 3 * HID * HID, ein_b[i],  (long)3 * HID * HID);
+            add(enc_out_w + (size_t)i * HID * HID,     eout_b[i], (long)HID * HID);
+            add(enc_l1_w  + (size_t)i * FFD * HID,     el1_b[i],  (long)FFD * HID);
+            add(enc_l2_w  + (size_t)i * HID * FFD,     el2_b[i],  (long)HID * FFD);
         }
-
-        cls_kernel<<<(R + 3) / 4, 256, 0, stream>>>(srcbuf, cls_w, cls_b, (float*)d_out, R);
-    }
-}
+        ca.n = k;
+        batch_cvt_kernel<<<b0, 256, 0, stream>>>(ca);
+    }
+
+    zero_prep_kernel<<<(Z + 2 * HID + 255) / 256, 256, 0, stream>>>(
+        zbase, Z, gat2_bl, gat2_br, bias2);
+    pass0_kernel<<<gE, 256, 0, stream>>>(edge_index, E, target_idx, L, cntE0, srcs0, f1);
+    compact_kernel<<<(Nn + 255) / 256, 256, 0, stream>>>(f1, map1, list1, cnt1, Nn);
+    pass1_kernel<<<gE, 256, 0, stream>>>(edge_index, E, f1, map1, cntE1, srcs1, f2);
+    compact_kernel<<<(Nn + 255) / 256, 256, 0, stream>>>(f2, map2, list2, cnt2, Nn);
+
+    gather2_kernel<<<2560, 256, 0, stream>>>(node_features, nf2c, list2, cnt2,
+                                             nf1c, list1, cnt1, DF);
+
+    {
+        GemmDesc gl = {nf2c, w1lT, gat1_bl, xlc, Nn,   HID, DF, 8, cnt2, 0, 1};
+        GemmDesc gr = {nf1c, w1rT, gat1_br, xrc, cap1, HID, DF, 8, cnt1, 0, 1};
+        int n0 = 8 * gMn2, n1 = 8 * gMn1;
+        gemm_dual_kernel<<<n0 + n1, 256, 0, stream>>>(gl, n0, gr, n1);
+    }
+    gat_wave1_kernel<<<cap1 / 4, 256, 0, stream>>>(
+        xlc, xrc, gat1_att, srcs1, cntE1, map2, cnt1, gat1_bias, x1c);
+
+    {
+        GemmDesc g2 = {x1c, w2T, bias2, x12c, cap1, 2 * HID, HID, 16, cnt1, 0, 1};
+        gemm_one_kernel<<<16 * gMn1, 256, 0, stream>>>(g2);
+    }
+    gat_wave2_kernel<<<(L + 3) / 4, 256, 0, stream>>>(
+        x12c, gat2_att, target_idx, L, srcs0, cntE0, map1, gat2_bias, x2c);
+
+    {
+        GemmDesc gv = {imgb, xa_v_b, xa_in_b + 2 * HID, vprojb, B, HID, HID, 8, nullptr, 0, 1};
+        gemm_one_kernel<<<8, 256, 0, stream>>>(gv);
+        GemmDesc go = {vprojb, xa_o_b, xa_out_b, attnb, B, HID, HID, 8, nullptr, 0, 0};
+        gemm_one_kernel<<<8, 256, 0, stream>>>(go);
+    }
+    ln_cross_kernel<<<R, 256, 0, stream>>>(x2c, attnb, xl_n1_g, xl_n1_b, srcbuf, srcb16, L);
+
+    gemm_bsk_kernel<4><<<dim3(FFD / 128, (R + 127) / 128, 4), 256, 0, stream>>>(
+        srcb16, xl1_b, skpart, R, FFD, HID);
+    sk_reduce_b16_kernel<1, 4><<<(int)(((long)R * FFD / 4 + 255) / 256), 256, 0, stream>>>(
+        skpart, xl_l1_b, h1b, (long)R * FFD, FFD);
+    gemm_bsk_kernel<8><<<dim3(HID / 128, (R + 127) / 128, 8), 256, 0, stream>>>(
+        h1b, xl2_b, skpart, R, HID, FFD);
+    sk_reduce_ln_kernel<8><<<R, 256, 0, stream>>>(
+        skpart, xl_l2_b, srcbuf, srcb16, xl_n2_g, xl_n2_b, MNr);
+
+    for (int i = 0; i < 2; ++i) {
+        gemm_bsk_kernel<4><<<dim3(3 * HID / 128, (R + 127) / 128, 4), 256, 0, stream>>>(
+            srcb16, ein_b[i], skpart, R, 3 * HID, HID);
+        self_attn_sk_kernel<4><<<B * 4, 256, 0, stream>>>(
+            skpart, enc_in_b + (size_t)i * 3 * HID, ffb16, L, R);
+        gemm_bsk_kernel<4><<<dim3(HID / 128, (R + 127) / 128, 4), 256, 0, stream>>>(
+            ffb16, eout_b[i], skpart, R, HID, HID);
+        sk_reduce_ln_kernel<4><<<R, 256, 0, stream>>>(
+            skpart, enc_out_b + (size_t)i * HID, srcbuf, srcb16,
+            enc_n1_g + (size_t)i * HID, enc_n1_b + (size_t)i * HID, MNr);
+        gemm_bsk_kernel<4><<<dim3(FFD / 128, (R + 127) / 128, 4), 256, 0, stream>>>(
+            srcb16, el1_b[i], skpart, R, FFD, HID);
+        sk_reduce_b16_kernel<1, 4><<<(int)(((long)R * FFD / 4 + 255) / 256), 256, 0, stream>>>(
+            skpart, enc_l1_b + (size_t)i * FFD, h1b, (long)R * FFD, FFD);
+        gemm_bsk_kernel<8><<<dim3(HID / 128, (R + 127) / 128, 8), 256, 0, stream>>>(
+            h1b, el2_b[i], skpart, R, HID, FFD);
+        sk_reduce_ln_kernel<8><<<R, 256, 0, stream>>>(
+            skpart, enc_l2_b + (size_t)i * HID, srcbuf, srcb16,
+            enc_n2_g + (size_t)i * HID, enc_n2_b + (size_t)i * HID, MNr);
+    }
+
+    cls_kernel<<<(R + 3) / 4, 256, 0, stream>>>(srcbuf, cls_w, cls_b, (float*)d_out, R);
+}
```
